# Optimization experiments

Measured on AMD Instinct MI355X. Metric: run time of the kernel, lower is better.

## Reference

```python
import jax, jax.numpy as jnp
import numpy as np

B = 262144
IN_FEATURES = 128
OUT_FEATURES = 128
NQ_IN = IN_FEATURES // 4
NQ_OUT = OUT_FEATURES // 4


def setup_inputs() -> dict:
    key = jax.random.key(0)
    kx, kw, kb = jax.random.split(key, 3)
    stdv = 1.0 / np.sqrt(IN_FEATURES).astype(np.float32)
    x = jax.random.normal(kx, (B, IN_FEATURES), dtype=jnp.float32)
    weight = jax.random.uniform(kw, (NQ_OUT, NQ_IN, 4), dtype=jnp.float32,
                                minval=-stdv, maxval=stdv)
    bias = jax.random.uniform(kb, (OUT_FEATURES,), dtype=jnp.float32,
                              minval=-stdv, maxval=stdv)
    return {"x": x, "weight": weight, "bias": bias}


def reference(x, weight, bias):
    b = x.shape[0]
    nq_in = weight.shape[1]
    # [B, nq_in, 4] quaternion components
    xq = x.reshape(b, nq_in, 4)
    xa, xi, xj, xk = xq[..., 0], xq[..., 1], xq[..., 2], xq[..., 3]
    wa, wi, wj, wk = weight[..., 0], weight[..., 1], weight[..., 2], weight[..., 3]
    # each term: [B, nq_in] @ [nq_in, nq_out] -> [B, nq_out]
    mm = lambda u, w: jnp.einsum('bn,on->bo', u, w)
    out_a = mm(xa, wa) - mm(xi, wi) - mm(xj, wj) - mm(xk, wk)
    out_i = mm(xa, wi) + mm(xi, wa) + mm(xj, wk) - mm(xk, wj)
    out_j = mm(xa, wj) - mm(xi, wk) + mm(xj, wa) + mm(xk, wi)
    out_k = mm(xa, wk) + mm(xi, wj) - mm(xj, wi) + mm(xk, wa)
    out = jnp.stack([out_a, out_i, out_j, out_k], axis=-1).reshape(b, -1)
    return out + bias
```

## Files before the change

kernel.cpp:

```cpp
#include <hip/hip_runtime.h>
#include <hip/hip_bf16.h>

typedef __bf16 bf16x8 __attribute__((ext_vector_type(8)));
typedef float  f32x4  __attribute__((ext_vector_type(4)));

#define NTILES 16384

__global__ __launch_bounds__(256) void prep_wfrag(const float* __restrict__ w,
                                                  ushort* __restrict__ wfrag) {
    int t = blockIdx.x * 256 + threadIdx.x;
    if (t >= 128 * 128) return;
    int j    = t & 7;
    int lane = (t >> 3) & 63;
    int kb   = (t >> 9) & 3;
    int nt   = t >> 11;
    int g    = lane >> 4;
    int n = nt * 16 + (lane & 15);
    int k = kb * 32 + (j < 4 ? g * 4 + j : 16 + g * 4 + (j - 4));
    int o  = n >> 2, c = n & 3;
    int nq = k >> 2, d = k & 3;
    int comp = c ^ d;
    bool neg = (d != 0) && ((c == 0) || (c != d && d != (c % 3) + 1));
    float val = w[o * 128 + nq * 4 + comp];
    val = neg ? -val : val;
    __bf16 bv = (__bf16)val;
    wfrag[t] = *reinterpret_cast<ushort*>(&bv);
}

__global__ __launch_bounds__(256, 4) void qgemm(const float* __restrict__ x,
                                                const ushort* __restrict__ wfrag,
                                                const float* __restrict__ bias,
                                                float* __restrict__ out) {
    __shared__ __align__(16) float stage[4][2048];

    int tid   = threadIdx.x;
    int lane  = tid & 63;
    int wid   = tid >> 6;
    int row16 = lane & 15;
    int kgrp  = lane >> 4;
    int loff  = row16 * 128 + kgrp * 4;

    size_t tile = (size_t)blockIdx.x * 4 + wid;
    const float4* xv = (const float4*)(x + tile * 2048 + loff);
    float4 r[8];
#pragma unroll
    for (int kb = 0; kb < 4; ++kb) {
        r[2 * kb]     = xv[kb * 8];
        r[2 * kb + 1] = xv[kb * 8 + 4];
    }

    bf16x8 afr[4];
#pragma unroll
    for (int kb = 0; kb < 4; ++kb) {
        float4 p = r[2 * kb], q = r[2 * kb + 1];
        afr[kb][0] = (__bf16)p.x; afr[kb][1] = (__bf16)p.y;
        afr[kb][2] = (__bf16)p.z; afr[kb][3] = (__bf16)p.w;
        afr[kb][4] = (__bf16)q.x; afr[kb][5] = (__bf16)q.y;
        afr[kb][6] = (__bf16)q.z; afr[kb][7] = (__bf16)q.w;
    }

    const bf16x8* wg = (const bf16x8*)wfrag;
    f32x4 acc[8];
#pragma unroll
    for (int nt = 0; nt < 8; ++nt) {
        acc[nt] = *(const f32x4*)(bias + nt * 16 + kgrp * 4);
#pragma unroll
        for (int kb = 0; kb < 4; ++kb) {
            bf16x8 wfr = wg[(nt * 4 + kb) * 64 + lane];
            acc[nt] = __builtin_amdgcn_mfma_f32_16x16x32_bf16(wfr, afr[kb], acc[nt], 0, 0, 0);
        }
    }

    float* stg = stage[wid];
#pragma unroll
    for (int nt = 0; nt < 8; ++nt) {
        int c = nt * 4 + kgrp;
        *(f32x4*)(stg + row16 * 128 + ((c ^ (row16 & 7)) << 2)) = acc[nt];
    }
    asm volatile("s_waitcnt lgkmcnt(0)" ::: "memory");
    __builtin_amdgcn_sched_barrier(0);

    f32x4* ob = (f32x4*)(out + tile * 2048);
#pragma unroll
    for (int s = 0; s < 8; ++s) {
        int p   = lane + 64 * s;
        int row = p >> 5;
        int c   = p & 31;
        f32x4 v = *(const f32x4*)(stg + row * 128 + ((c ^ (row & 7)) << 2));
        __builtin_nontemporal_store(v, ob + p);
    }
}

extern "C" void kernel_launch(void* const* d_in, const int* in_sizes, int n_in,
                              void* d_out, int out_size, void* d_ws, size_t ws_size,
                              hipStream_t stream) {
    const float* x      = (const float*)d_in[0];
    const float* weight = (const float*)d_in[1];
    const float* bias   = (const float*)d_in[2];
    float*       out    = (float*)d_out;
    ushort*      wfrag  = (ushort*)d_ws;

    prep_wfrag<<<64, 256, 0, stream>>>(weight, wfrag);
    qgemm<<<4096, 256, 0, stream>>>(x, wfrag, bias, out);
}
```

Before: 58.17 us.

## Make GEMM persistent with weights in registers and double-buffered async LDS loads

The grid shrinks from 4096 to 256 blocks, and each wave now processes 16 tiles in sequence. All weight fragments and biases are held in registers across tiles. Input tiles are prefetched two ahead into a per-wave LDS double buffer with global_load_lds, and each buffer is reused as the output staging area. This is meant to hide load latency and remove repeated weight loads, at the cost of occupancy dropping to one block per CU. It also depends on hand-tuned vmcnt counts being correct.

```diff
diff --git a/kernel.cpp b/kernel.cpp
--- a/kernel.cpp
+++ b/kernel.cpp
@@ -4,7 +4,8 @@
 typedef __bf16 bf16x8 __attribute__((ext_vector_type(8)));
 typedef float  f32x4  __attribute__((ext_vector_type(4)));
 
-#define NTILES 16384
+#define NT_PER_WAVE 16
+#define GEMM_BLOCKS 256
 
 __global__ __launch_bounds__(256) void prep_wfrag(const float* __restrict__ w,
                                                   ushort* __restrict__ wfrag) {
@@ -27,67 +28,102 @@
     wfrag[t] = *reinterpret_cast<ushort*>(&bv);
 }
 
-__global__ __launch_bounds__(256, 4) void qgemm(const float* __restrict__ x,
+__global__ __launch_bounds__(256, 1) void qgemm(const float* __restrict__ x,
                                                 const ushort* __restrict__ wfrag,
                                                 const float* __restrict__ bias,
                                                 float* __restrict__ out) {
-    __shared__ __align__(16) float stage[4][2048];
+    __shared__ __align__(16) float xring[4][2][2048];
 
     int tid   = threadIdx.x;
     int lane  = tid & 63;
     int wid   = tid >> 6;
     int row16 = lane & 15;
     int kgrp  = lane >> 4;
-    int loff  = row16 * 128 + kgrp * 4;
-
-    size_t tile = (size_t)blockIdx.x * 4 + wid;
-    const float4* xv = (const float4*)(x + tile * 2048 + loff);
-    float4 r[8];
-#pragma unroll
-    for (int kb = 0; kb < 4; ++kb) {
-        r[2 * kb]     = xv[kb * 8];
-        r[2 * kb + 1] = xv[kb * 8 + 4];
-    }
-
-    bf16x8 afr[4];
-#pragma unroll
-    for (int kb = 0; kb < 4; ++kb) {
-        float4 p = r[2 * kb], q = r[2 * kb + 1];
-        afr[kb][0] = (__bf16)p.x; afr[kb][1] = (__bf16)p.y;
-        afr[kb][2] = (__bf16)p.z; afr[kb][3] = (__bf16)p.w;
-        afr[kb][4] = (__bf16)q.x; afr[kb][5] = (__bf16)q.y;
-        afr[kb][6] = (__bf16)q.z; afr[kb][7] = (__bf16)q.w;
-    }
 
     const bf16x8* wg = (const bf16x8*)wfrag;
-    f32x4 acc[8];
+    bf16x8 wreg[32];
 #pragma unroll
-    for (int nt = 0; nt < 8; ++nt) {
-        acc[nt] = *(const f32x4*)(bias + nt * 16 + kgrp * 4);
+    for (int f = 0; f < 32; ++f) wreg[f] = wg[f * 64 + lane];
+
+    f32x4 bv[8];
+#pragma unroll
+    for (int nt = 0; nt < 8; ++nt) bv[nt] = *(const f32x4*)(bias + nt * 16 + kgrp * 4);
+
+    size_t tile0 = ((size_t)blockIdx.x * 4 + wid) * NT_PER_WAVE;
+    float* buf0 = xring[wid][0];
+    float* buf1 = xring[wid][1];
+
+    auto stage = [&](float* buf, size_t t) {
+        const char* tb = (const char*)(x + t * 2048);
+#pragma unroll
+        for (int I = 0; I < 8; ++I) {
+            int s  = I * 64 + lane;
+            int rr = s >> 5;
+            int pc = s & 31;
+            int gc = rr * 32 + ((pc - 2 * rr) & 31);
+            __builtin_amdgcn_global_load_lds(
+                (const __attribute__((address_space(1))) void*)(tb + gc * 16),
+                (__attribute__((address_space(3))) void*)(buf + I * 256),
+                16, 0, 0);
+        }
+    };
+
+    stage(buf0, tile0);
+    stage(buf1, tile0 + 1);
+
+#pragma unroll
+    for (int i = 0; i < NT_PER_WAVE; ++i) {
+        float* cur = (i & 1) ? buf1 : buf0;
+
+        if (i == 0 || i == NT_PER_WAVE - 1)
+            asm volatile("s_waitcnt vmcnt(8)" ::: "memory");
+        else
+            asm volatile("s_waitcnt vmcnt(16)" ::: "memory");
+        __builtin_amdgcn_sched_barrier(0);
+
+        bf16x8 afr[4];
 #pragma unroll
         for (int kb = 0; kb < 4; ++kb) {
-            bf16x8 wfr = wg[(nt * 4 + kb) * 64 + lane];
-            acc[nt] = __builtin_amdgcn_mfma_f32_16x16x32_bf16(wfr, afr[kb], acc[nt], 0, 0, 0);
+            int c1 = 8 * kb + kgrp;
+            int c2 = 8 * kb + 4 + kgrp;
+            f32x4 lo = *(const f32x4*)(cur + row16 * 128 + (((c1 + 2 * row16) & 31) << 2));
+            f32x4 hi = *(const f32x4*)(cur + row16 * 128 + (((c2 + 2 * row16) & 31) << 2));
+            afr[kb][0] = (__bf16)lo[0]; afr[kb][1] = (__bf16)lo[1];
+            afr[kb][2] = (__bf16)lo[2]; afr[kb][3] = (__bf16)lo[3];
+            afr[kb][4] = (__bf16)hi[0]; afr[kb][5] = (__bf16)hi[1];
+            afr[kb][6] = (__bf16)hi[2]; afr[kb][7] = (__bf16)hi[3];
         }
-    }
 
-    float* stg = stage[wid];
+        f32x4 acc[8];
 #pragma unroll
-    for (int nt = 0; nt < 8; ++nt) {
-        int c = nt * 4 + kgrp;
-        *(f32x4*)(stg + row16 * 128 + ((c ^ (row16 & 7)) << 2)) = acc[nt];
-    }
-    asm volatile("s_waitcnt lgkmcnt(0)" ::: "memory");
-    __builtin_amdgcn_sched_barrier(0);
+        for (int nt = 0; nt < 8; ++nt) {
+            acc[nt] = bv[nt];
+#pragma unroll
+            for (int kb = 0; kb < 4; ++kb)
+                acc[nt] = __builtin_amdgcn_mfma_f32_16x16x32_bf16(wreg[nt * 4 + kb], afr[kb], acc[nt], 0, 0, 0);
+        }
 
-    f32x4* ob = (f32x4*)(out + tile * 2048);
 #pragma unroll
-    for (int s = 0; s < 8; ++s) {
-        int p   = lane + 64 * s;
-        int row = p >> 5;
-        int c   = p & 31;
-        f32x4 v = *(const f32x4*)(stg + row * 128 + ((c ^ (row & 7)) << 2));
-        __builtin_nontemporal_store(v, ob + p);
+        for (int nt = 0; nt < 8; ++nt) {
+            int c = nt * 4 + kgrp;
+            *(f32x4*)(cur + row16 * 128 + ((c ^ (row16 & 7)) << 2)) = acc[nt];
+        }
+        asm volatile("s_waitcnt lgkmcnt(0)" ::: "memory");
+        __builtin_amdgcn_sched_barrier(0);
+
+        f32x4* ob = (f32x4*)(out + (tile0 + i) * 2048);
+#pragma unroll
+        for (int s = 0; s < 8; ++s) {
+            int p   = lane + 64 * s;
+            int row = p >> 5;
+            int c   = p & 31;
+            f32x4 v = *(const f32x4*)(cur + row * 128 + ((c ^ (row & 7)) << 2));
+            __builtin_nontemporal_store(v, ob + p);
+        }
+        __builtin_amdgcn_sched_barrier(0);
+
+        if (i + 2 < NT_PER_WAVE) stage(cur, tile0 + i + 2);
+        __builtin_amdgcn_sched_barrier(0);
     }
 }
 
@@ -101,5 +137,5 @@
     ushort*      wfrag  = (ushort*)d_ws;
 
     prep_wfrag<<<64, 256, 0, stream>>>(weight, wfrag);
-    qgemm<<<4096, 256, 0, stream>>>(x, wfrag, bias, out);
+    qgemm<<<GEMM_BLOCKS, 256, 0, stream>>>(x, wfrag, bias, out);
 }
```

New measurement: 50.88 us. -12.5%, faster.
